# Performance work log

Hardware: AMD Instinct MI355X
Metric: run time of the kernel (lower is better)

## Reference

```python
import jax, jax.numpy as jnp
import numpy as np

N_HEAD, D_K, D_V = 8, 64, 64
TOPK = 16
B, N_R, N_W = 256, 64, 64
D_READ = D_WRITE = D_OUT = 512
TEMP = float(np.power(D_K, 0.5))
EPS = 1e-7  # 10e-8 in original Sparse_attention


def sparse_attention(a, top_k):
    # a: (rows, n); RIMs Sparse_attention: threshold at k-th largest, clamp, renormalize
    if a.shape[-1] <= top_k:
        return a
    delta = jax.lax.top_k(a, top_k)[0][..., -1:] + EPS
    w = jnp.clip(a - delta, 0.0, None)
    return w / (jnp.sum(w, axis=-1, keepdims=True) + EPS)


def setup_inputs() -> dict:
    key = jax.random.key(0)
    ks = jax.random.split(key, 8)
    q = jax.random.normal(ks[0], (B, N_R, D_READ), dtype=jnp.float32)
    k = jax.random.normal(ks[1], (B, N_W, D_WRITE), dtype=jnp.float32)
    v = jax.random.normal(ks[2], (B, N_W, D_WRITE), dtype=jnp.float32)
    # GroupLinearLayer weights: (num_blocks, d_in, n_head*d)
    Wq = 0.02 * jax.random.normal(ks[3], (N_R, D_READ, N_HEAD * D_K), dtype=jnp.float32)
    Wk = 0.02 * jax.random.normal(ks[4], (N_W, D_WRITE, N_HEAD * D_K), dtype=jnp.float32)
    Wv = 0.02 * jax.random.normal(ks[5], (N_W, D_WRITE, N_HEAD * D_V), dtype=jnp.float32)
    fc_w = 0.02 * jax.random.normal(ks[6], (D_OUT, N_HEAD * D_V), dtype=jnp.float32)
    fc_b = jnp.zeros((D_OUT,), dtype=jnp.float32)
    gate_w = 0.02 * jax.random.normal(ks[7], (D_OUT, N_HEAD * D_V), dtype=jnp.float32)
    gate_b = jnp.zeros((D_OUT,), dtype=jnp.float32)
    return {"q": q, "k": k, "v": v, "Wq": Wq, "Wk": Wk, "Wv": Wv,
            "fc_w": fc_w, "fc_b": fc_b, "gate_w": gate_w, "gate_b": gate_b}


def reference(q, k, v, Wq, Wk, Wv, fc_w, fc_b, gate_w, gate_b):
    # grouped per-block projections: out[b,n] = x[b,n] @ W[n]
    qp = jnp.einsum('bnd,nde->bne', q, Wq).reshape(B, N_R, N_HEAD, D_K)
    kp = jnp.einsum('bnd,nde->bne', k, Wk).reshape(B, N_W, N_HEAD, D_K)
    vp = jnp.einsum('bnd,nde->bne', v, Wv).reshape(B, N_W, N_HEAD, D_V)
    # (H*B, len, d) with head-major leading dim, matching permute(2,0,1,3).view(-1,...)
    qh = qp.transpose(2, 0, 1, 3).reshape(N_HEAD * B, N_R, D_K)
    kh = kp.transpose(2, 0, 1, 3).reshape(N_HEAD * B, N_W, D_K)
    vh = vp.transpose(2, 0, 1, 3).reshape(N_HEAD * B, N_W, D_V)
    scores = jnp.einsum('ijk,ilk->ijl', qh, kh) / TEMP          # (HB, Nr, Nw)
    a = jnp.exp(jnp.max(scores, axis=-1, keepdims=True))        # (HB, Nr, 1)
    # flag=True: softmax over the query-block dim (permute/softmax/reshape)
    a = jax.nn.softmax(a[..., 0], axis=-1)                      # (HB, Nr)
    a = sparse_attention(a, TOPK)                               # (HB, Nr)
    attn = a[..., None]                                         # (HB, Nr, 1)
    # einsum 'ijk,ikl->ijl' with attn's k-dim == 1 broadcasts: attn * sum_k v
    out = attn * jnp.sum(vh, axis=1, keepdims=True)             # (HB, Nr, Dv)
    out = out.reshape(N_HEAD, B, N_R, D_V).transpose(1, 2, 0, 3).reshape(B, N_R, N_HEAD * D_V)
    fc_out = out @ fc_w.T + fc_b
    gate = jax.nn.sigmoid(out @ gate_w.T + gate_b)
    output = gate * jnp.tanh(fc_out)                            # residual=True gating
    return output
```

## Files before the change

kernel.cpp:

```cpp
#include <hip/hip_runtime.h>
#include <stdint.h>

#define B_    256
#define NR    64
#define NW    64
#define DIN   512
#define NH    8
#define DK    64
#define E_    512
#define TEMP_INV 0.125f
#define EPSV  1e-7f

typedef unsigned short u16;
typedef unsigned int   u32;
typedef _Float16 f16;
typedef __attribute__((ext_vector_type(2))) float    floatx2;
typedef __attribute__((ext_vector_type(4))) float    floatx4;
typedef __attribute__((ext_vector_type(4))) u32      uintx4;
typedef __attribute__((ext_vector_type(2))) _Float16 halfx2;
typedef __attribute__((ext_vector_type(8))) _Float16 halfx8;

__device__ __forceinline__ u32 asu(float f) { union { float f; u32 u; } c; c.f = f; return c.u; }
__device__ __forceinline__ halfx2 h2(u32 u) { union { u32 u; halfx2 h; } c; c.u = u; return c.h; }
__device__ __forceinline__ u32 pkh(float a, float b) {
    union { halfx2 h; u32 u; } c; c.h = (halfx2){(f16)a, (f16)b}; return c.u;
}

#if __has_builtin(__builtin_amdgcn_fdot2)
#define FDOT2(a, b, c) __builtin_amdgcn_fdot2((a), (b), (c), false)
#else
__device__ __forceinline__ float FDOT2(halfx2 a, halfx2 b, float c) {
    return fmaf((float)a.y, (float)b.y, fmaf((float)a.x, (float)b.x, c));
}
#endif

__global__ __launch_bounds__(256)
void proj_kernel(const float* __restrict__ q, const float* __restrict__ kk_,
                 const float* __restrict__ v,
                 const float* __restrict__ Wq, const float* __restrict__ Wk,
                 const float* __restrict__ Wv,
                 f16* __restrict__ qp, f16* __restrict__ kp,
                 float* __restrict__ vsum)
{
    const float* X; const float* W; f16* dst = nullptr; bool vmode = false;
    if (blockIdx.z == 0)      { X = q;   W = Wq; dst = qp; }
    else if (blockIdx.z == 1) { X = kk_; W = Wk; dst = kp; }
    else                      { X = v;   W = Wv; vmode = true; }

    const int n  = blockIdx.x * 8 + (blockIdx.y & 7);
    const int t  = blockIdx.y >> 3;
    const int m0 = (t >> 2) * 128;
    const int n0 = (t & 3) * 128;

    __shared__ u16 As[4096];
    __shared__ u16 Bs[4096];

    const int tid  = threadIdx.x;
    const int lane = tid & 63;
    const int wave = tid >> 6;
    const int wm   = (wave >> 1) * 64;
    const int wn   = (wave & 1) * 64;
    const int l15  = lane & 15;
    const int quad = lane >> 4;

    floatx4 acc[4][4];
#pragma unroll
    for (int i = 0; i < 4; i++)
#pragma unroll
        for (int j = 0; j < 4; j++) acc[i][j] = (floatx4){0.f, 0.f, 0.f, 0.f};

    const int arow  = tid >> 1;
    const int ahalf = tid & 1;
    const float* aptr = X + ((size_t)(m0 + arow) * NW + n) * DIN + ahalf * 16;
    const int kq = tid >> 6;
    const int p  = tid & 63;
    const float* wptr = W + (size_t)n * (DIN * E_) + n0 + 2 * p;

    floatx4 pa[4]; floatx2 pb[8];
#pragma unroll
    for (int c = 0; c < 4; c++) pa[c] = *(const floatx4*)(aptr + c * 4);
#pragma unroll
    for (int j = 0; j < 8; j++) pb[j] = *(const floatx2*)(wptr + (size_t)(kq * 8 + j) * E_);

    for (int it = 0; it < 16; it++) {
        {
            u32 h[8];
#pragma unroll
            for (int c = 0; c < 4; c++) {
                h[2 * c]     = pkh(pa[c].x, pa[c].y);
                h[2 * c + 1] = pkh(pa[c].z, pa[c].w);
            }
            *(uintx4*)&As[(2 * ahalf + 0) * 1024 + arow * 8] = (uintx4){h[0], h[1], h[2], h[3]};
            *(uintx4*)&As[(2 * ahalf + 1) * 1024 + arow * 8] = (uintx4){h[4], h[5], h[6], h[7]};
        }
#pragma unroll
        for (int eo = 0; eo < 2; eo++) {
            uintx4 hv = (uintx4){pkh(pb[0][eo], pb[1][eo]), pkh(pb[2][eo], pb[3][eo]),
                                 pkh(pb[4][eo], pb[5][eo]), pkh(pb[6][eo], pb[7][eo])};
            *(uintx4*)&Bs[kq * 1024 + eo * 512 + p * 8] = hv;
        }

        if (it < 15) {
            const int kn = it * 32 + 32;
#pragma unroll
            for (int c = 0; c < 4; c++) pa[c] = *(const floatx4*)(aptr + kn + c * 4);
#pragma unroll
            for (int j = 0; j < 8; j++)
                pb[j] = *(const floatx2*)(wptr + (size_t)(kn + kq * 8 + j) * E_);
        }

        __syncthreads();

        halfx8 af[4], bf[4];
#pragma unroll
        for (int mi = 0; mi < 4; mi++) {
            int R = wm + mi * 16 + l15;
            af[mi] = *(const halfx8*)&As[quad * 1024 + R * 8];
        }
#pragma unroll
        for (int ni = 0; ni < 4; ni++) {
            int e = wn + ni * 16 + l15;
            bf[ni] = *(const halfx8*)&Bs[quad * 1024 + (e & 1) * 512 + (e >> 1) * 8];
        }
#pragma unroll
        for (int mi = 0; mi < 4; mi++)
#pragma unroll
            for (int ni = 0; ni < 4; ni++)
                acc[mi][ni] = __builtin_amdgcn_mfma_f32_16x16x32_f16(
                    af[mi], bf[ni], acc[mi][ni], 0, 0, 0);
        __syncthreads();
    }

    if (!vmode) {
#pragma unroll
        for (int mi = 0; mi < 4; mi++) {
            int rowb = m0 + wm + mi * 16 + quad * 4;
#pragma unroll
            for (int ni = 0; ni < 4; ni++) {
                int col = n0 + wn + ni * 16 + l15;
#pragma unroll
                for (int r = 0; r < 4; r++)
                    dst[((size_t)(rowb + r) * NW + n) * E_ + col] = (f16)acc[mi][ni][r];
            }
        }
    } else {
#pragma unroll
        for (int mi = 0; mi < 4; mi++) {
            int rowb = m0 + wm + mi * 16 + quad * 4;
#pragma unroll
            for (int ni = 0; ni < 4; ni++) {
                int col = n0 + wn + ni * 16 + l15;
#pragma unroll
                for (int r = 0; r < 4; r++)
                    atomicAdd(&vsum[(size_t)(rowb + r) * E_ + col], acc[mi][ni][r]);
            }
        }
    }
}

__global__ __launch_bounds__(256)
void attn_kernel(const f16* __restrict__ qp, const f16* __restrict__ kp,
                 float* __restrict__ attnT)
{
    const int h = blockIdx.x >> 8;
    const int b = blockIdx.x & 255;
    __shared__ float mred[4][64];

    const int t    = threadIdx.x;
    const int w    = t >> 6;
    const int lane = t & 63;

    const f16* qrow = qp + ((size_t)(b * NR + lane)) * E_ + h * DK;
    halfx2 qreg[32];
#pragma unroll
    for (int c = 0; c < 8; c++) {
        uintx4 u = *(const uintx4*)(qrow + c * 8);
        qreg[c * 4 + 0] = h2(u.x); qreg[c * 4 + 1] = h2(u.y);
        qreg[c * 4 + 2] = h2(u.z); qreg[c * 4 + 3] = h2(u.w);
    }

    float m = -1e30f;
    for (int ll = 0; ll < 16; ll++) {
        int lu = __builtin_amdgcn_readfirstlane(w * 16 + ll);
        const u32* k32 = (const u32*)(kp + ((size_t)(b * NW + lu)) * E_ + h * DK);
        float a0 = 0.f, a1 = 0.f;
#pragma unroll
        for (int c = 0; c < 32; c += 2) {
            a0 = FDOT2(qreg[c],     h2(k32[c]),     a0);
            a1 = FDOT2(qreg[c + 1], h2(k32[c + 1]), a1);
        }
        m = fmaxf(m, a0 + a1);
    }
    mred[w][lane] = m;
    __syncthreads();

    if (t < 64) {
        float mm = fmaxf(fmaxf(mred[0][lane], mred[1][lane]),
                         fmaxf(mred[2][lane], mred[3][lane])) * TEMP_INV;
        float e = expf(mm);
        float mx = e;
#pragma unroll
        for (int d = 1; d < 64; d <<= 1) mx = fmaxf(mx, __shfl_xor(mx, d));
        float tt = expf(e - mx);
        float S = tt;
#pragma unroll
        for (int d = 1; d < 64; d <<= 1) S += __shfl_xor(S, d);
        float s = tt / S;

        float cur = s, v16 = 0.f;
        for (int itk = 0; itk < 16; itk++) {
            float mv = cur;
#pragma unroll
            for (int d = 1; d < 64; d <<= 1) mv = fmaxf(mv, __shfl_xor(mv, d));
            unsigned long long bal = __ballot(cur == mv);
            int first = __ffsll(bal) - 1;
            if (lane == first) cur = -1e30f;
            v16 = mv;
        }
        float delta = v16 + EPSV;
        float ww = fmaxf(s - delta, 0.f);
        float sw = ww;
#pragma unroll
        for (int d = 1; d < 64; d <<= 1) sw += __shfl_xor(sw, d);
        attnT[((size_t)b * NR + lane) * NH + h] = ww / (sw + EPSV);
    }
}

__global__ __launch_bounds__(256)
void fcv_kernel(const float* __restrict__ vsum, const float* __restrict__ fc_w,
                const float* __restrict__ gate_w, float* __restrict__ fcv,
                float* __restrict__ gatev)
{
    const int ohalf = blockIdx.x >> 3;
    const int bq    = blockIdx.x & 7;
    const int h     = blockIdx.y;
    const float* W  = blockIdx.z ? gate_w : fc_w;
    float* out      = blockIdx.z ? gatev : fcv;
    const int o     = ohalf * 256 + threadIdx.x;

    __shared__ float vs[32 * 64];
#pragma unroll
    for (int i = 0; i < 8; i++) {
        int idx = i * 256 + threadIdx.x;
        int bb = idx >> 6, d = idx & 63;
        vs[idx] = vsum[(size_t)(bq * 32 + bb) * E_ + h * DK + d];
    }
    floatx4 wr[16];
#pragma unroll
    for (int c = 0; c < 16; c++)
        wr[c] = *(const floatx4*)(W + (size_t)o * E_ + h * DK + c * 4);
    __syncthreads();

    for (int bb = 0; bb < 32; bb++) {
        const floatx4* vr = (const floatx4*)&vs[bb * 64];
        float a = 0.f;
#pragma unroll
        for (int c = 0; c < 16; c++) {
            floatx4 vv = vr[c];
            a += vv.x * wr[c].x + vv.y * wr[c].y + vv.z * wr[c].z + vv.w * wr[c].w;
        }
        out[((size_t)(bq * 32 + bb) * NH + h) * E_ + o] = a;
    }
}

__global__ __launch_bounds__(256)
void final_kernel(const float* __restrict__ fcv, const float* __restrict__ gatev,
                  const float* __restrict__ attnT, const float* __restrict__ fc_b,
                  const float* __restrict__ gate_b, float* __restrict__ out)
{
    const int b = blockIdx.x;
    const int tid = threadIdx.x;
    __shared__ float ats[NR * NH];

    ats[tid]       = attnT[(size_t)b * NR * NH + tid];
    ats[256 + tid] = attnT[(size_t)b * NR * NH + 256 + tid];

    float fr[2][8], gr[2][8];
#pragma unroll
    for (int half = 0; half < 2; half++) {
        int o = half * 256 + tid;
#pragma unroll
        for (int hh = 0; hh < 8; hh++) {
            fr[half][hh] = fcv[((size_t)b * NH + hh) * E_ + o];
            gr[half][hh] = gatev[((size_t)b * NH + hh) * E_ + o];
        }
    }
    float bfc0 = fc_b[tid],   bfc1 = fc_b[256 + tid];
    float bgt0 = gate_b[tid], bgt1 = gate_b[256 + tid];
    __syncthreads();

    for (int r = 0; r < NR; r++) {
        float a[8];
#pragma unroll
        for (int hh = 0; hh < 8; hh++) a[hh] = ats[r * NH + hh];
#pragma unroll
        for (int half = 0; half < 2; half++) {
            int o = half * 256 + tid;
            float fc = half ? bfc1 : bfc0;
            float gt = half ? bgt1 : bgt0;
#pragma unroll
            for (int hh = 0; hh < 8; hh++) {
                fc = fmaf(a[hh], fr[half][hh], fc);
                gt = fmaf(a[hh], gr[half][hh], gt);
            }
            float g  = 1.f / (1.f + __expf(-gt));
            float e2 = __expf(2.f * fc);
            float th = 1.f - 2.f / (e2 + 1.f);
            out[((size_t)(b * NR + r)) * E_ + o] = g * th;
        }
    }
}

extern "C" void kernel_launch(void* const* d_in, const int* in_sizes, int n_in,
                              void* d_out, int out_size, void* d_ws, size_t ws_size,
                              hipStream_t stream)
{
    const float* q      = (const float*)d_in[0];
    const float* k      = (const float*)d_in[1];
    const float* v      = (const float*)d_in[2];
    const float* Wq     = (const float*)d_in[3];
    const float* Wk     = (const float*)d_in[4];
    const float* Wv     = (const float*)d_in[5];
    const float* fc_w   = (const float*)d_in[6];
    const float* fc_b   = (const float*)d_in[7];
    const float* gate_w = (const float*)d_in[8];
    const float* gate_b = (const float*)d_in[9];
    float* out = (float*)d_out;

    char* ws = (char*)d_ws;
    f16*   qp    = (f16*)(ws);
    f16*   kp    = (f16*)(ws + 16777216);
    float* vsum  = (float*)(ws + 33554432);
    float* attnT = (float*)(ws + 33554432 + 524288);
    float* fcv   = (float*)(ws + 33554432 + 2 * 524288);
    float* gatev = (float*)(ws + 33554432 + 2 * 524288 + 4194304);

    hipMemsetAsync(vsum, 0, 524288, stream);

    hipLaunchKernelGGL(proj_kernel, dim3(8, 64, 3), dim3(256), 0, stream,
                       q, k, v, Wq, Wk, Wv, qp, kp, vsum);
    hipLaunchKernelGGL(attn_kernel, dim3(2048), dim3(256), 0, stream, qp, kp, attnT);
    hipLaunchKernelGGL(fcv_kernel, dim3(16, 8, 2), dim3(256), 0, stream,
                       vsum, fc_w, gate_w, fcv, gatev);
    hipLaunchKernelGGL(final_kernel, dim3(256), dim3(256), 0, stream,
                       fcv, gatev, attnT, fc_b, gate_b, out);
}
```

Before: 381.0 us.

## Double-buffer projection GEMM, use MFMA for attention scores, split vsum and final kernels

The projection GEMM now double-buffers its LDS tiles and loads W two k-steps ahead, so global loads overlap with MFMA compute. When the workspace is large enough, V projections are written as fp16 and summed by a separate kernel, which replaces the global float atomics and the memset. The attention score computation moves from per-lane fdot2 loops to MFMA on tiles staged in LDS. The final kernel is split across four row groups per batch to raise parallelism. The costs are twice the LDS use in the projection kernel, an extra fp16 write and read of V, and an extra kernel launch.

```diff
diff --git a/kernel.cpp b/kernel.cpp
--- a/kernel.cpp
+++ b/kernel.cpp
@@ -20,19 +20,65 @@
 typedef __attribute__((ext_vector_type(2))) _Float16 halfx2;
 typedef __attribute__((ext_vector_type(8))) _Float16 halfx8;
 
-__device__ __forceinline__ u32 asu(float f) { union { float f; u32 u; } c; c.f = f; return c.u; }
 __device__ __forceinline__ halfx2 h2(u32 u) { union { u32 u; halfx2 h; } c; c.u = u; return c.h; }
 __device__ __forceinline__ u32 pkh(float a, float b) {
     union { halfx2 h; u32 u; } c; c.h = (halfx2){(f16)a, (f16)b}; return c.u;
 }
 
-#if __has_builtin(__builtin_amdgcn_fdot2)
-#define FDOT2(a, b, c) __builtin_amdgcn_fdot2((a), (b), (c), false)
-#else
-__device__ __forceinline__ float FDOT2(halfx2 a, halfx2 b, float c) {
-    return fmaf((float)a.y, (float)b.y, fmaf((float)a.x, (float)b.x, c));
-}
-#endif
+
+#define STORE_A(sbuf) do {                                                    \
+        u32 hh_[8];                                                           \
+        _Pragma("unroll")                                                     \
+        for (int c = 0; c < 4; c++) {                                         \
+            hh_[2*c]   = pkh(pa[c].x, pa[c].y);                               \
+            hh_[2*c+1] = pkh(pa[c].z, pa[c].w);                               \
+        }                                                                     \
+        *(uintx4*)&As[sbuf][(2*ahalf+0)*1024 + arow*8] =                      \
+            (uintx4){hh_[0],hh_[1],hh_[2],hh_[3]};                            \
+        *(uintx4*)&As[sbuf][(2*ahalf+1)*1024 + arow*8] =                      \
+            (uintx4){hh_[4],hh_[5],hh_[6],hh_[7]};                            \
+    } while (0)
+
+#define STORE_B(sbuf, pb) do {                                                \
+        _Pragma("unroll")                                                     \
+        for (int eo = 0; eo < 2; eo++) {                                      \
+            uintx4 hv_ = (uintx4){pkh(pb[0][eo], pb[1][eo]),                  \
+                                  pkh(pb[2][eo], pb[3][eo]),                  \
+                                  pkh(pb[4][eo], pb[5][eo]),                  \
+                                  pkh(pb[6][eo], pb[7][eo])};                 \
+            *(uintx4*)&Bs[sbuf][kq*1024 + eo*512 + p*8] = hv_;                \
+        }                                                                     \
+    } while (0)
+
+#define LOAD_A(kn) do {                                                       \
+        _Pragma("unroll")                                                     \
+        for (int c = 0; c < 4; c++)                                           \
+            pa[c] = *(const floatx4*)(aptr + (kn) + c * 4);                   \
+    } while (0)
+
+#define LOAD_B(pb, kn) do {                                                   \
+        _Pragma("unroll")                                                     \
+        for (int j = 0; j < 8; j++)                                           \
+            pb[j] = *(const floatx2*)(wptr + (size_t)((kn) + kq*8 + j) * E_); \
+    } while (0)
+
+#define COMPUTE(sbuf) do {                                                    \
+        halfx8 af_[4], bf_[4];                                                \
+        _Pragma("unroll")                                                     \
+        for (int mi = 0; mi < 4; mi++)                                        \
+            af_[mi] = *(const halfx8*)&As[sbuf][quad*1024 + (wm + mi*16 + l15)*8]; \
+        _Pragma("unroll")                                                     \
+        for (int ni = 0; ni < 4; ni++) {                                      \
+            int e_ = wn + ni*16 + l15;                                        \
+            bf_[ni] = *(const halfx8*)&Bs[sbuf][quad*1024 + (e_&1)*512 + (e_>>1)*8]; \
+        }                                                                     \
+        _Pragma("unroll")                                                     \
+        for (int mi = 0; mi < 4; mi++)                                        \
+            _Pragma("unroll")                                                 \
+            for (int ni = 0; ni < 4; ni++)                                    \
+                acc[mi][ni] = __builtin_amdgcn_mfma_f32_16x16x32_f16(         \
+                    af_[mi], bf_[ni], acc[mi][ni], 0, 0, 0);                  \
+    } while (0)
 
 __global__ __launch_bounds__(256)
 void proj_kernel(const float* __restrict__ q, const float* __restrict__ kk_,
@@ -40,20 +86,20 @@
                  const float* __restrict__ Wq, const float* __restrict__ Wk,
                  const float* __restrict__ Wv,
                  f16* __restrict__ qp, f16* __restrict__ kp,
-                 float* __restrict__ vsum)
-{
-    const float* X; const float* W; f16* dst = nullptr; bool vmode = false;
+                 f16* __restrict__ vp, float* __restrict__ vsum)
+{
+    const float* X; const float* W; f16* dst;
     if (blockIdx.z == 0)      { X = q;   W = Wq; dst = qp; }
     else if (blockIdx.z == 1) { X = kk_; W = Wk; dst = kp; }
-    else                      { X = v;   W = Wv; vmode = true; }
+    else                      { X = v;   W = Wv; dst = vp; }
 
     const int n  = blockIdx.x * 8 + (blockIdx.y & 7);
-    const int t  = blockIdx.y >> 3;
-    const int m0 = (t >> 2) * 128;
-    const int n0 = (t & 3) * 128;
-
-    __shared__ u16 As[4096];
-    __shared__ u16 Bs[4096];
+    const int t_ = blockIdx.y >> 3;
+    const int m0 = (t_ >> 2) * 128;
+    const int n0 = (t_ & 3) * 128;
+
+    __shared__ u16 As[2][4096];
+    __shared__ u16 Bs[2][4096];
 
     const int tid  = threadIdx.x;
     const int lane = tid & 63;
@@ -76,62 +122,30 @@
     const int p  = tid & 63;
     const float* wptr = W + (size_t)n * (DIN * E_) + n0 + 2 * p;
 
-    floatx4 pa[4]; floatx2 pb[8];
-#pragma unroll
-    for (int c = 0; c < 4; c++) pa[c] = *(const floatx4*)(aptr + c * 4);
-#pragma unroll
-    for (int j = 0; j < 8; j++) pb[j] = *(const floatx2*)(wptr + (size_t)(kq * 8 + j) * E_);
-
-    for (int it = 0; it < 16; it++) {
-        {
-            u32 h[8];
-#pragma unroll
-            for (int c = 0; c < 4; c++) {
-                h[2 * c]     = pkh(pa[c].x, pa[c].y);
-                h[2 * c + 1] = pkh(pa[c].z, pa[c].w);
-            }
-            *(uintx4*)&As[(2 * ahalf + 0) * 1024 + arow * 8] = (uintx4){h[0], h[1], h[2], h[3]};
-            *(uintx4*)&As[(2 * ahalf + 1) * 1024 + arow * 8] = (uintx4){h[4], h[5], h[6], h[7]};
-        }
-#pragma unroll
-        for (int eo = 0; eo < 2; eo++) {
-            uintx4 hv = (uintx4){pkh(pb[0][eo], pb[1][eo]), pkh(pb[2][eo], pb[3][eo]),
-                                 pkh(pb[4][eo], pb[5][eo]), pkh(pb[6][eo], pb[7][eo])};
-            *(uintx4*)&Bs[kq * 1024 + eo * 512 + p * 8] = hv;
-        }
-
-        if (it < 15) {
-            const int kn = it * 32 + 32;
-#pragma unroll
-            for (int c = 0; c < 4; c++) pa[c] = *(const floatx4*)(aptr + kn + c * 4);
-#pragma unroll
-            for (int j = 0; j < 8; j++)
-                pb[j] = *(const floatx2*)(wptr + (size_t)(kn + kq * 8 + j) * E_);
-        }
-
+    floatx4 pa[4];
+    floatx2 pb0[8], pb1[8];
+
+    LOAD_A(0);
+    LOAD_B(pb0, 0);
+    LOAD_B(pb1, 32);
+
+#pragma unroll 1
+    for (int it2 = 0; it2 < 8; it2++) {
+        const int k0 = it2 * 64;
+        STORE_A(0);
+        STORE_B(0, pb0);
+        LOAD_A(k0 + 32);
+        if (it2 < 7) { LOAD_B(pb0, k0 + 64); }
         __syncthreads();
-
-        halfx8 af[4], bf[4];
-#pragma unroll
-        for (int mi = 0; mi < 4; mi++) {
-            int R = wm + mi * 16 + l15;
-            af[mi] = *(const halfx8*)&As[quad * 1024 + R * 8];
-        }
-#pragma unroll
-        for (int ni = 0; ni < 4; ni++) {
-            int e = wn + ni * 16 + l15;
-            bf[ni] = *(const halfx8*)&Bs[quad * 1024 + (e & 1) * 512 + (e >> 1) * 8];
-        }
-#pragma unroll
-        for (int mi = 0; mi < 4; mi++)
-#pragma unroll
-            for (int ni = 0; ni < 4; ni++)
-                acc[mi][ni] = __builtin_amdgcn_mfma_f32_16x16x32_f16(
-                    af[mi], bf[ni], acc[mi][ni], 0, 0, 0);
+        COMPUTE(0);
+        STORE_A(1);
+        STORE_B(1, pb1);
+        if (it2 < 7) { LOAD_A(k0 + 64); LOAD_B(pb1, k0 + 96); }
         __syncthreads();
-    }
-
-    if (!vmode) {
+        COMPUTE(1);
+    }
+
+    if (dst) {
 #pragma unroll
         for (int mi = 0; mi < 4; mi++) {
             int rowb = m0 + wm + mi * 16 + quad * 4;
@@ -159,44 +173,75 @@
 }
 
 __global__ __launch_bounds__(256)
+void vsum_kernel(const f16* __restrict__ vp, float* __restrict__ vsum)
+{
+    const int b = blockIdx.x;
+    const int t = threadIdx.x;
+    const u32* src = (const u32*)vp + (size_t)b * NW * (E_ / 2) + t;
+    float s0 = 0.f, s1 = 0.f;
+#pragma unroll 4
+    for (int nn = 0; nn < NW; nn++) {
+        halfx2 hv = h2(src[(size_t)nn * (E_ / 2)]);
+        s0 += (float)hv.x;
+        s1 += (float)hv.y;
+    }
+    *(floatx2*)&vsum[(size_t)b * E_ + 2 * t] = (floatx2){s0, s1};
+}
+
+__global__ __launch_bounds__(256)
 void attn_kernel(const f16* __restrict__ qp, const f16* __restrict__ kp,
                  float* __restrict__ attnT)
 {
     const int h = blockIdx.x >> 8;
     const int b = blockIdx.x & 255;
-    __shared__ float mred[4][64];
+    __shared__ u16 qs[64 * 72];
+    __shared__ u16 ks[64 * 72];
+    __shared__ float ms[64];
 
     const int t    = threadIdx.x;
     const int w    = t >> 6;
     const int lane = t & 63;
-
-    const f16* qrow = qp + ((size_t)(b * NR + lane)) * E_ + h * DK;
-    halfx2 qreg[32];
-#pragma unroll
-    for (int c = 0; c < 8; c++) {
-        uintx4 u = *(const uintx4*)(qrow + c * 8);
-        qreg[c * 4 + 0] = h2(u.x); qreg[c * 4 + 1] = h2(u.y);
-        qreg[c * 4 + 2] = h2(u.z); qreg[c * 4 + 3] = h2(u.w);
-    }
-
-    float m = -1e30f;
-    for (int ll = 0; ll < 16; ll++) {
-        int lu = __builtin_amdgcn_readfirstlane(w * 16 + ll);
-        const u32* k32 = (const u32*)(kp + ((size_t)(b * NW + lu)) * E_ + h * DK);
-        float a0 = 0.f, a1 = 0.f;
-#pragma unroll
-        for (int c = 0; c < 32; c += 2) {
-            a0 = FDOT2(qreg[c],     h2(k32[c]),     a0);
-            a1 = FDOT2(qreg[c + 1], h2(k32[c + 1]), a1);
-        }
-        m = fmaxf(m, a0 + a1);
-    }
-    mred[w][lane] = m;
+    const int l15  = lane & 15;
+    const int quad = lane >> 4;
+
+    {
+        const int r = t >> 2, c = t & 3;
+        const f16* qsrc = qp + ((size_t)(b * NR + r)) * E_ + h * DK + c * 16;
+        const f16* ksrc = kp + ((size_t)(b * NW + r)) * E_ + h * DK + c * 16;
+        *(uintx4*)&qs[r * 72 + c * 16]     = *(const uintx4*)(qsrc);
+        *(uintx4*)&qs[r * 72 + c * 16 + 8] = *(const uintx4*)(qsrc + 8);
+        *(uintx4*)&ks[r * 72 + c * 16]     = *(const uintx4*)(ksrc);
+        *(uintx4*)&ks[r * 72 + c * 16 + 8] = *(const uintx4*)(ksrc + 8);
+    }
     __syncthreads();
 
+    floatx4 sc[4];
+#pragma unroll
+    for (int ni = 0; ni < 4; ni++) sc[ni] = (floatx4){0.f, 0.f, 0.f, 0.f};
+
+    halfx8 af[2];
+#pragma unroll
+    for (int kk = 0; kk < 2; kk++)
+        af[kk] = *(const halfx8*)&qs[(w * 16 + l15) * 72 + kk * 32 + quad * 8];
+#pragma unroll
+    for (int ni = 0; ni < 4; ni++)
+#pragma unroll
+        for (int kk = 0; kk < 2; kk++) {
+            halfx8 bf = *(const halfx8*)&ks[(ni * 16 + l15) * 72 + kk * 32 + quad * 8];
+            sc[ni] = __builtin_amdgcn_mfma_f32_16x16x32_f16(af[kk], bf, sc[ni], 0, 0, 0);
+        }
+
+#pragma unroll
+    for (int r = 0; r < 4; r++) {
+        float rm = fmaxf(fmaxf(sc[0][r], sc[1][r]), fmaxf(sc[2][r], sc[3][r]));
+#pragma unroll
+        for (int d = 1; d < 16; d <<= 1) rm = fmaxf(rm, __shfl_xor(rm, d));
+        if (l15 == 0) ms[w * 16 + quad * 4 + r] = rm;
+    }
+    __syncthreads();
+
     if (t < 64) {
-        float mm = fmaxf(fmaxf(mred[0][lane], mred[1][lane]),
-                         fmaxf(mred[2][lane], mred[3][lane])) * TEMP_INV;
+        float mm = ms[lane] * TEMP_INV;
         float e = expf(mm);
         float mx = e;
 #pragma unroll
@@ -268,12 +313,12 @@
                   const float* __restrict__ attnT, const float* __restrict__ fc_b,
                   const float* __restrict__ gate_b, float* __restrict__ out)
 {
-    const int b = blockIdx.x;
+    const int b   = blockIdx.x;
+    const int r0  = blockIdx.y * 16;
     const int tid = threadIdx.x;
-    __shared__ float ats[NR * NH];
-
-    ats[tid]       = attnT[(size_t)b * NR * NH + tid];
-    ats[256 + tid] = attnT[(size_t)b * NR * NH + 256 + tid];
+    __shared__ float ats[16 * NH];
+
+    if (tid < 16 * NH) ats[tid] = attnT[(size_t)b * NR * NH + r0 * NH + tid];
 
     float fr[2][8], gr[2][8];
 #pragma unroll
@@ -289,7 +334,7 @@
     float bgt0 = gate_b[tid], bgt1 = gate_b[256 + tid];
     __syncthreads();
 
-    for (int r = 0; r < NR; r++) {
+    for (int r = 0; r < 16; r++) {
         float a[8];
 #pragma unroll
         for (int hh = 0; hh < 8; hh++) a[hh] = ats[r * NH + hh];
@@ -306,7 +351,7 @@
             float g  = 1.f / (1.f + __expf(-gt));
             float e2 = __expf(2.f * fc);
             float th = 1.f - 2.f / (e2 + 1.f);
-            out[((size_t)(b * NR + r)) * E_ + o] = g * th;
+            out[((size_t)(b * NR + r0 + r)) * E_ + o] = g * th;
         }
     }
 }
@@ -328,20 +373,33 @@
     float* out = (float*)d_out;
 
     char* ws = (char*)d_ws;
-    f16*   qp    = (f16*)(ws);
-    f16*   kp    = (f16*)(ws + 16777216);
-    float* vsum  = (float*)(ws + 33554432);
-    float* attnT = (float*)(ws + 33554432 + 524288);
-    float* fcv   = (float*)(ws + 33554432 + 2 * 524288);
-    float* gatev = (float*)(ws + 33554432 + 2 * 524288 + 4194304);
-
-    hipMemsetAsync(vsum, 0, 524288, stream);
+    f16* qp = (f16*)(ws);
+    f16* kp = (f16*)(ws + (16u << 20));
+
+    const bool big = ws_size >= (50u << 20);
+    f16* vp; float* vsum; float* attnT; float* fcv; float* gatev;
+    if (big) {
+        vp    = (f16*)(ws + (32u << 20));
+        vsum  = (float*)(ws + (48u << 20));
+        attnT = (float*)(ws + (48u << 20) + 524288);
+        fcv   = (float*)(ws + (32u << 20));
+        gatev = (float*)(ws + (36u << 20));
+    } else {
+        vp    = nullptr;
+        vsum  = (float*)(ws + 33554432);
+        attnT = (float*)(ws + 33554432 + 524288);
+        fcv   = (float*)(ws + 33554432 + 2 * 524288);
+        gatev = (float*)(ws + 33554432 + 2 * 524288 + 4194304);
+        hipMemsetAsync(vsum, 0, 524288, stream);
+    }
 
     hipLaunchKernelGGL(proj_kernel, dim3(8, 64, 3), dim3(256), 0, stream,
-                       q, k, v, Wq, Wk, Wv, qp, kp, vsum);
+                       q, k, v, Wq, Wk, Wv, qp, kp, vp, vsum);
     hipLaunchKernelGGL(attn_kernel, dim3(2048), dim3(256), 0, stream, qp, kp, attnT);
+    if (big)
+        hipLaunchKernelGGL(vsum_kernel, dim3(256), dim3(256), 0, stream, vp, vsum);
     hipLaunchKernelGGL(fcv_kernel, dim3(16, 8, 2), dim3(256), 0, stream,
                        vsum, fc_w, gate_w, fcv, gatev);
-    hipLaunchKernelGGL(final_kernel, dim3(256), dim3(256), 0, stream,
+    hipLaunchKernelGGL(final_kernel, dim3(256, 4), dim3(256), 0, stream,
                        fcv, gatev, attnT, fc_b, gate_b, out);
 }
```

Measured after the change: 355.8 us. 6.6% less time.
